# Optimization experiments

Measured on AMD Instinct MI355X. Metric: run time of the kernel, lower is better.

## Reference

```python
import jax, jax.numpy as jnp
import numpy as np

D = 128
SCALE = 1.0 / np.sqrt(D)  # scalar_value


def setup_inputs() -> dict:
    key = jax.random.key(0)
    k1, k2, k3 = jax.random.split(key, 3)
    B, N, S = 2, 16, 2048
    q = jax.random.normal(k1, (B, N, S, D), dtype=jnp.float32)
    k = jax.random.normal(k2, (B, N, S, D), dtype=jnp.float32)
    v = jax.random.normal(k3, (B, N, S, D), dtype=jnp.float32)
    return {"q": q, "k": k, "v": v}


def reference(q, k, v):
    # BNSD layout. scores = scale * Q K^T, causal mask, softmax with
    # explicit max/sum tracking (golden for NPU fusion attention).
    s1, s2 = q.shape[2], k.shape[2]
    scores = jnp.einsum('bnsd,bntd->bnst', q, k) * SCALE
    # generate_attn_mask: causal (lower-triangular kept), masked -> -inf
    causal = jnp.triu(jnp.ones((s1, s2), dtype=bool), k=1)
    scores = jnp.where(causal, -jnp.inf, scores)
    softmax_max = jnp.max(scores, axis=-1, keepdims=True)          # [B,N,S,1]
    exp_scores = jnp.exp(scores - softmax_max)
    softmax_sum = jnp.sum(exp_scores, axis=-1, keepdims=True)      # [B,N,S,1]
    softmax_res = exp_scores / softmax_sum
    out = jnp.einsum('bnst,bntd->bnsd', softmax_res, v)
    # NPU golden repeats stats x8 along last dim
    return (out,
            jnp.tile(softmax_max, (1, 1, 1, 8)),
            jnp.tile(softmax_sum, (1, 1, 1, 8)))
```

## Files before the change

kernel.cpp:

```cpp
#include <hip/hip_runtime.h>
#include <math.h>
#include <stdint.h>

#define D_DIM 128
#define SEQ 2048
#define NHEADS 32
#define BC 64
#define SCALE 0.08838834764831843f
#define IMG_U16 24576

typedef short bf16x8 __attribute__((ext_vector_type(8)));
typedef float f32x4 __attribute__((ext_vector_type(4)));

union Frag { uint32_t u[4]; bf16x8 v; unsigned short s[8]; };
union Pack8 { unsigned short s[8]; uint4 q; };

__device__ __forceinline__ uint32_t fbits(float x) { return __builtin_bit_cast(uint32_t, x); }
__device__ __forceinline__ float bbits(uint32_t u) { return __builtin_bit_cast(float, u); }
__device__ __forceinline__ unsigned short bf16_rne(float x) {
    uint32_t u = fbits(x);
    u += 0x7FFFu + ((u >> 16) & 1u);
    return (unsigned short)(u >> 16);
}
__device__ __forceinline__ void split2(float a, float b, uint32_t& hp, uint32_t& lp) {
    uint32_t ua = fbits(a) & 0xFFFF0000u, ub = fbits(b) & 0xFFFF0000u;
    float la = a - bbits(ua), lb = b - bbits(ub);
    hp = (ua >> 16) | ub;
    lp = (fbits(la) >> 16) | (fbits(lb) & 0xFFFF0000u);
}

__device__ __forceinline__ void gl_lds16(const unsigned short* g, unsigned short* l) {
    __builtin_amdgcn_global_load_lds(
        (const __attribute__((address_space(1))) uint32_t*)g,
        (__attribute__((address_space(3))) uint32_t*)l, 16, 0, 0);
}

__global__ __launch_bounds__(256) void cvt_kv(
    const float* __restrict__ k, const float* __restrict__ v, unsigned short* __restrict__ ws)
{
    const int b = blockIdx.x;
    const int h = b >> 5, jt = b & 31;
    const int t = (int)threadIdx.x;
    unsigned short* img = ws + (size_t)b * IMG_U16;
    const float* kp = k + ((size_t)h * SEQ + jt * 64) * D_DIM;
    const float* vp = v + ((size_t)h * SEQ + jt * 64) * D_DIM;

    #pragma unroll
    for (int u = 0; u < 4; ++u) {
        int idx = u * 256 + t;
        int n = idx >> 4, kc8 = idx & 15;
        float e[8];
        *(float4*)(e)     = *(const float4*)(kp + (size_t)n * D_DIM + kc8 * 8);
        *(float4*)(e + 4) = *(const float4*)(kp + (size_t)n * D_DIM + kc8 * 8 + 4);
        uint32_t hp[4], lp[4];
        #pragma unroll
        for (int j = 0; j < 4; ++j) split2(e[2 * j], e[2 * j + 1], hp[j], lp[j]);
        int off = n * 128 + ((kc8 ^ (n & 7)) * 8);
        *(uint4*)(img + off)        = make_uint4(hp[0], hp[1], hp[2], hp[3]);
        *(uint4*)(img + 8192 + off) = make_uint4(lp[0], lp[1], lp[2], lp[3]);
    }
    #pragma unroll
    for (int u = 0; u < 4; ++u) {
        int idx = u * 256 + t;
        int d = idx >> 3, cc = idx & 7;
        Pack8 p8;
        #pragma unroll
        for (int j = 0; j < 8; ++j)
            p8.s[j] = bf16_rne(vp[(size_t)(cc * 8 + j) * D_DIM + d]);
        int off = d * 64 + ((cc ^ (d & 7)) * 8);
        *(uint4*)(img + 16384 + off) = p8.q;
    }
}

__global__ __launch_bounds__(512, 2) void fa_fwd3(
    const float* __restrict__ q, const unsigned short* __restrict__ ws, float* __restrict__ out)
{
    __shared__ __align__(16) unsigned short Stage[2][IMG_U16];
    __shared__ __align__(16) unsigned short Pbs[128 * 64];

    const int x = blockIdx.x;
    const int it = 15 - (x >> 5);
    const int h = x & 31;

    const int t    = (int)threadIdx.x;
    const int wb   = t >> 6;
    const int lane = t & 63;
    const int ln   = lane & 15;
    const int qd   = lane >> 4;

    const unsigned short* wsh = ws + (size_t)(h * 32) * IMG_U16;
    float* out_o = out;
    float* out_m = out + (size_t)NHEADS * SEQ * D_DIM;
    float* out_l = out_m + (size_t)NHEADS * SEQ * 8;

    const int qrow0 = it * 128 + wb * 16;

    {
        const unsigned short* g = wsh + wb * 3072 + lane * 8;
        unsigned short* l = &Stage[0][wb * 3072];
        #pragma unroll
        for (int i = 0; i < 6; ++i) gl_lds16(g + i * 512, l + i * 512);
    }

    Frag Qh[4], Ql[4];
    {
        const float* qp = q + ((size_t)h * SEQ + qrow0 + ln) * D_DIM;
        #pragma unroll
        for (int kc = 0; kc < 4; ++kc) {
            const int kb = kc * 32 + qd * 8;
            float e[8];
            *(float4*)(e)     = *(const float4*)(qp + kb);
            *(float4*)(e + 4) = *(const float4*)(qp + kb + 4);
            #pragma unroll
            for (int j = 0; j < 4; ++j)
                split2(e[2 * j], e[2 * j + 1], Qh[kc].u[j], Ql[kc].u[j]);
        }
    }

    f32x4 accO[8];
    float m_r[4], l_r[4];
    #pragma unroll
    for (int nd = 0; nd < 8; ++nd) accO[nd] = (f32x4){0.f, 0.f, 0.f, 0.f};
    #pragma unroll
    for (int r = 0; r < 4; ++r) { m_r[r] = -INFINITY; l_r[r] = 0.f; }

    const int jt_end = 2 * it + 1;
    for (int jt = 0; jt <= jt_end; ++jt) {
        const int c0 = jt * BC;
        __syncthreads();

        if (jt < jt_end) {
            const unsigned short* g = wsh + (size_t)(jt + 1) * IMG_U16 + wb * 3072 + lane * 8;
            unsigned short* l = &Stage[(jt + 1) & 1][wb * 3072];
            #pragma unroll
            for (int i = 0; i < 6; ++i) gl_lds16(g + i * 512, l + i * 512);
        }

        const unsigned short* Khs = Stage[jt & 1];
        const unsigned short* Kls = Khs + 8192;
        const unsigned short* Vhs = Khs + 16384;

        if (c0 <= qrow0 + 15) {
            f32x4 accS[4];
            #pragma unroll
            for (int nt = 0; nt < 4; ++nt) accS[nt] = (f32x4){0.f, 0.f, 0.f, 0.f};
            #pragma unroll
            for (int kc = 0; kc < 4; ++kc) {
                #pragma unroll
                for (int nt = 0; nt < 4; ++nt) {
                    int n = nt * 16 + ln;
                    int off = n * 128 + (((kc * 4 + qd) ^ (n & 7)) * 8);
                    Frag Bh, Bl;
                    Bh.v = *(const bf16x8*)(Khs + off);
                    Bl.v = *(const bf16x8*)(Kls + off);
                    f32x4 c = accS[nt];
                    c = __builtin_amdgcn_mfma_f32_16x16x32_bf16(Qh[kc].v, Bh.v, c, 0, 0, 0);
                    c = __builtin_amdgcn_mfma_f32_16x16x32_bf16(Qh[kc].v, Bl.v, c, 0, 0, 0);
                    c = __builtin_amdgcn_mfma_f32_16x16x32_bf16(Ql[kc].v, Bh.v, c, 0, 0, 0);
                    accS[nt] = c;
                }
            }
            #pragma unroll
            for (int r = 0; r < 4; ++r) {
                const int rowg = qrow0 + qd * 4 + r;
                float sv[4], mx = -INFINITY;
                #pragma unroll
                for (int nt = 0; nt < 4; ++nt) {
                    float s = accS[nt][r] * SCALE;
                    if (c0 + nt * 16 + ln > rowg) s = -INFINITY;
                    sv[nt] = s; mx = fmaxf(mx, s);
                }
                #pragma unroll
                for (int off = 1; off < 16; off <<= 1) mx = fmaxf(mx, __shfl_xor(mx, off));
                const float mnew = fmaxf(m_r[r], mx);
                const float alpha = __expf(m_r[r] - mnew);
                float p[4], rs = 0.f;
                #pragma unroll
                for (int nt = 0; nt < 4; ++nt) { p[nt] = __expf(sv[nt] - mnew); rs += p[nt]; }
                #pragma unroll
                for (int off = 1; off < 16; off <<= 1) rs += __shfl_xor(rs, off);
                m_r[r] = mnew;
                l_r[r] = l_r[r] * alpha + rs;
                #pragma unroll
                for (int nd = 0; nd < 8; ++nd) accO[nd][r] *= alpha;
                const int R = wb * 16 + qd * 4 + r;
                #pragma unroll
                for (int nt = 0; nt < 4; ++nt) {
                    int c = nt * 16 + ln;
                    Pbs[R * 64 + (((c >> 3) ^ (R & 7)) * 8) + (c & 7)] = bf16_rne(p[nt]);
                }
            }
            #pragma unroll
            for (int kc2 = 0; kc2 < 2; ++kc2) {
                Frag Pf;
                const int R = wb * 16 + ln;
                Pf.v = *(const bf16x8*)(Pbs + R * 64 + (((kc2 * 4 + qd) ^ (R & 7)) * 8));
                #pragma unroll
                for (int nd = 0; nd < 8; ++nd) {
                    int dcol = nd * 16 + ln;
                    int voff = dcol * 64 + (((kc2 * 4 + qd) ^ (dcol & 7)) * 8);
                    Frag Vh2;
                    Vh2.v = *(const bf16x8*)(Vhs + voff);
                    accO[nd] = __builtin_amdgcn_mfma_f32_16x16x32_bf16(Pf.v, Vh2.v, accO[nd], 0, 0, 0);
                }
            }
        }
    }

    #pragma unroll
    for (int r = 0; r < 4; ++r) {
        const int rowg = qrow0 + qd * 4 + r;
        const float invl = 1.0f / l_r[r];
        float* op = out_o + (size_t)h * SEQ * D_DIM + (size_t)rowg * D_DIM;
        #pragma unroll
        for (int nd = 0; nd < 8; ++nd) op[nd * 16 + ln] = accO[nd][r] * invl;
        if (ln < 8) {
            size_t sb = ((size_t)h * SEQ + rowg) * 8 + ln;
            out_m[sb] = m_r[r];
            out_l[sb] = l_r[r];
        }
    }
}

__global__ __launch_bounds__(256, 2) void fa_fwd_fb(
    const float* __restrict__ q, const float* __restrict__ k,
    const float* __restrict__ v, float* __restrict__ out)
{
    __shared__ __align__(16) unsigned short Khs[64 * 128];
    __shared__ __align__(16) unsigned short Kls[64 * 128];
    __shared__ __align__(16) unsigned short Vhs[128 * 64];
    __shared__ __align__(16) unsigned short Vls[128 * 64];
    __shared__ __align__(16) unsigned short Pbs[128 * 64];

    const int x = blockIdx.x;
    const int y = x >> 3;
    const int s_idx = y & 15;
    const int h = (x & 7) * 4 + (y >> 4);
    const int it = (y < 32) ? (15 - s_idx) : s_idx;

    const int t = (int)threadIdx.x;
    const int wb = t >> 6, lane = t & 63, ln = lane & 15, qd = lane >> 4;

    const float* qh = q + (size_t)h * SEQ * D_DIM;
    const float* kh = k + (size_t)h * SEQ * D_DIM;
    const float* vh = v + (size_t)h * SEQ * D_DIM;
    float* out_o = out;
    float* out_m = out + (size_t)NHEADS * SEQ * D_DIM;
    float* out_l = out_m + (size_t)NHEADS * SEQ * 8;

    const int qrow0 = it * 128 + wb * 32;

    Frag Qh[2][4], Ql[2][4];
    #pragma unroll
    for (int mt = 0; mt < 2; ++mt) {
        const float* qp = qh + (size_t)(qrow0 + mt * 16 + ln) * D_DIM;
        #pragma unroll
        for (int kc = 0; kc < 4; ++kc) {
            const int kb = kc * 32 + qd * 8;
            float e[8];
            *(float4*)(e)     = *(const float4*)(qp + kb);
            *(float4*)(e + 4) = *(const float4*)(qp + kb + 4);
            #pragma unroll
            for (int j = 0; j < 4; ++j)
                split2(e[2 * j], e[2 * j + 1], Qh[mt][kc].u[j], Ql[mt][kc].u[j]);
        }
    }

    f32x4 accO[2][8];
    float m_r[2][4], l_r[2][4];
    #pragma unroll
    for (int mt = 0; mt < 2; ++mt) {
        #pragma unroll
        for (int nd = 0; nd < 8; ++nd) accO[mt][nd] = (f32x4){0.f, 0.f, 0.f, 0.f};
        #pragma unroll
        for (int r = 0; r < 4; ++r) { m_r[mt][r] = -INFINITY; l_r[mt][r] = 0.f; }
    }

    const int jt_end = 2 * it + 1;
    for (int jt = 0; jt <= jt_end; ++jt) {
        const int c0 = jt * BC;
        __syncthreads();
        #pragma unroll
        for (int itr = 0; itr < 8; ++itr) {
            int f = itr * 256 + t;
            int row = f >> 5, d4 = f & 31;
            float e[4];
            *(float4*)e = *(const float4*)(kh + (size_t)(c0 + row) * D_DIM + d4 * 4);
            uint32_t hp[2], lp[2];
            split2(e[0], e[1], hp[0], lp[0]);
            split2(e[2], e[3], hp[1], lp[1]);
            int off = row * 128 + (((d4 >> 1) ^ (row & 7)) * 8) + (d4 & 1) * 4;
            *(uint2*)(Khs + off) = make_uint2(hp[0], hp[1]);
            *(uint2*)(Kls + off) = make_uint2(lp[0], lp[1]);
        }
        #pragma unroll
        for (int uu = 0; uu < 4; ++uu) {
            int ug = wb * 4 + uu;
            int cc = ug >> 1, dh = ug & 1;
            int d = dh * 64 + lane;
            Frag fh, fl;
            #pragma unroll
            for (int j = 0; j < 8; j += 2) {
                float a = vh[(size_t)(c0 + cc * 8 + j) * D_DIM + d];
                float b = vh[(size_t)(c0 + cc * 8 + j + 1) * D_DIM + d];
                split2(a, b, fh.u[j >> 1], fl.u[j >> 1]);
            }
            int off = d * 64 + ((cc ^ (d & 7)) * 8);
            *(bf16x8*)(Vhs + off) = fh.v;
            *(bf16x8*)(Vls + off) = fl.v;
        }
        __syncthreads();

        if (c0 <= qrow0 + 31) {
            f32x4 accS[2][4];
            #pragma unroll
            for (int mt = 0; mt < 2; ++mt)
                #pragma unroll
                for (int nt = 0; nt < 4; ++nt) accS[mt][nt] = (f32x4){0.f, 0.f, 0.f, 0.f};
            #pragma unroll
            for (int kc = 0; kc < 4; ++kc) {
                #pragma unroll
                for (int ntp = 0; ntp < 4; ntp += 2) {
                    Frag Bh[2], Bl[2];
                    #pragma unroll
                    for (int e2 = 0; e2 < 2; ++e2) {
                        int n = (ntp + e2) * 16 + ln;
                        int off = n * 128 + (((kc * 4 + qd) ^ (n & 7)) * 8);
                        Bh[e2].v = *(const bf16x8*)(Khs + off);
                        Bl[e2].v = *(const bf16x8*)(Kls + off);
                    }
                    #pragma unroll
                    for (int mt = 0; mt < 2; ++mt)
                        #pragma unroll
                        for (int e2 = 0; e2 < 2; ++e2) {
                            f32x4 c = accS[mt][ntp + e2];
                            c = __builtin_amdgcn_mfma_f32_16x16x32_bf16(Qh[mt][kc].v, Bh[e2].v, c, 0, 0, 0);
                            c = __builtin_amdgcn_mfma_f32_16x16x32_bf16(Qh[mt][kc].v, Bl[e2].v, c, 0, 0, 0);
                            c = __builtin_amdgcn_mfma_f32_16x16x32_bf16(Ql[mt][kc].v, Bh[e2].v, c, 0, 0, 0);
                            accS[mt][ntp + e2] = c;
                        }
                }
            }
            #pragma unroll
            for (int mt = 0; mt < 2; ++mt) {
                #pragma unroll
                for (int r = 0; r < 4; ++r) {
                    const int rowg = qrow0 + mt * 16 + qd * 4 + r;
                    float sv[4], mx = -INFINITY;
                    #pragma unroll
                    for (int nt = 0; nt < 4; ++nt) {
                        float s = accS[mt][nt][r] * SCALE;
                        if (c0 + nt * 16 + ln > rowg) s = -INFINITY;
                        sv[nt] = s; mx = fmaxf(mx, s);
                    }
                    #pragma unroll
                    for (int off = 1; off < 16; off <<= 1) mx = fmaxf(mx, __shfl_xor(mx, off));
                    const float mnew = fmaxf(m_r[mt][r], mx);
                    const float alpha = __expf(m_r[mt][r] - mnew);
                    float p[4], rs = 0.f;
                    #pragma unroll
                    for (int nt = 0; nt < 4; ++nt) { p[nt] = __expf(sv[nt] - mnew); rs += p[nt]; }
                    #pragma unroll
                    for (int off = 1; off < 16; off <<= 1) rs += __shfl_xor(rs, off);
                    m_r[mt][r] = mnew;
                    l_r[mt][r] = l_r[mt][r] * alpha + rs;
                    #pragma unroll
                    for (int nd = 0; nd < 8; ++nd) accO[mt][nd][r] *= alpha;
                    const int R = wb * 32 + mt * 16 + qd * 4 + r;
                    #pragma unroll
                    for (int nt = 0; nt < 4; ++nt) {
                        int c = nt * 16 + ln;
                        Pbs[R * 64 + (((c >> 3) ^ (R & 7)) * 8) + (c & 7)] = bf16_rne(p[nt]);
                    }
                }
            }
            #pragma unroll
            for (int kc2 = 0; kc2 < 2; ++kc2) {
                Frag Pf[2];
                #pragma unroll
                for (int mt = 0; mt < 2; ++mt) {
                    int R = wb * 32 + mt * 16 + ln;
                    Pf[mt].v = *(const bf16x8*)(Pbs + R * 64 + (((kc2 * 4 + qd) ^ (R & 7)) * 8));
                }
                #pragma unroll
                for (int nd = 0; nd < 8; ++nd) {
                    int dcol = nd * 16 + ln;
                    int voff = dcol * 64 + (((kc2 * 4 + qd) ^ (dcol & 7)) * 8);
                    Frag Vh2, Vl2;
                    Vh2.v = *(const bf16x8*)(Vhs + voff);
                    Vl2.v = *(const bf16x8*)(Vls + voff);
                    #pragma unroll
                    for (int mt = 0; mt < 2; ++mt) {
                        f32x4 c = accO[mt][nd];
                        c = __builtin_amdgcn_mfma_f32_16x16x32_bf16(Pf[mt].v, Vh2.v, c, 0, 0, 0);
                        c = __builtin_amdgcn_mfma_f32_16x16x32_bf16(Pf[mt].v, Vl2.v, c, 0, 0, 0);
                        accO[mt][nd] = c;
                    }
                }
            }
        }
    }

    #pragma unroll
    for (int mt = 0; mt < 2; ++mt) {
        #pragma unroll
        for (int r = 0; r < 4; ++r) {
            const int rowg = qrow0 + mt * 16 + qd * 4 + r;
            const float invl = 1.0f / l_r[mt][r];
            float* op = out_o + (size_t)h * SEQ * D_DIM + (size_t)rowg * D_DIM;
            #pragma unroll
            for (int nd = 0; nd < 8; ++nd) op[nd * 16 + ln] = accO[mt][nd][r] * invl;
            if (ln < 8) {
                size_t sb = ((size_t)h * SEQ + rowg) * 8 + ln;
                out_m[sb] = m_r[mt][r];
                out_l[sb] = l_r[mt][r];
            }
        }
    }
}

extern "C" void kernel_launch(void* const* d_in, const int* in_sizes, int n_in,
                              void* d_out, int out_size, void* d_ws, size_t ws_size,
                              hipStream_t stream) {
    const float* q = (const float*)d_in[0];
    const float* k = (const float*)d_in[1];
    const float* v = (const float*)d_in[2];
    float* out = (float*)d_out;

    const size_t need = (size_t)1024 * IMG_U16 * sizeof(unsigned short);
    if (ws_size >= need) {
        unsigned short* ws = (unsigned short*)d_ws;
        cvt_kv<<<dim3(1024), dim3(256), 0, stream>>>(k, v, ws);
        fa_fwd3<<<dim3(512), dim3(512), 0, stream>>>(q, ws, out);
    } else {
        fa_fwd_fb<<<dim3(512), dim3(256), 0, stream>>>(q, k, v, out);
    }
}
```

Measured before the change: 246.2 us.

## Rework attention forward: 32 rows per wave, MFMA row sums, DPP max, LDS-transposed V

Each wave now handles two 16-row Q tiles, so every K/V fragment read from LDS feeds twice as many MFMAs, and the block shrinks to 256 threads. The K/V tile double buffer is dropped for a single buffer loaded synchronously with an extra barrier each step. Row sums now come from an MFMA against a ones vector instead of shuffle reductions, and the row max uses DPP. Query tiles are reordered so heavy and light causal blocks are interleaved. The V transpose in cvt_kv now goes through LDS so global reads are coalesced. The costs are more register pressure and no overlap between the K/V load and compute.

Measured after the change: 252.0 us. +2.4%, slower.

```diff
diff --git a/kernel.cpp b/kernel.cpp
--- a/kernel.cpp
+++ b/kernel.cpp
@@ -35,9 +35,23 @@
         (__attribute__((address_space(3))) uint32_t*)l, 16, 0, 0);
 }
 
+__device__ __forceinline__ float dpp_max16(float x) {
+    int y;
+    y = __builtin_amdgcn_update_dpp(0, __builtin_bit_cast(int, x), 0xB1, 0xF, 0xF, true);
+    x = fmaxf(x, __builtin_bit_cast(float, y));
+    y = __builtin_amdgcn_update_dpp(0, __builtin_bit_cast(int, x), 0x4E, 0xF, 0xF, true);
+    x = fmaxf(x, __builtin_bit_cast(float, y));
+    y = __builtin_amdgcn_update_dpp(0, __builtin_bit_cast(int, x), 0x141, 0xF, 0xF, true);
+    x = fmaxf(x, __builtin_bit_cast(float, y));
+    y = __builtin_amdgcn_update_dpp(0, __builtin_bit_cast(int, x), 0x140, 0xF, 0xF, true);
+    x = fmaxf(x, __builtin_bit_cast(float, y));
+    return x;
+}
+
 __global__ __launch_bounds__(256) void cvt_kv(
     const float* __restrict__ k, const float* __restrict__ v, unsigned short* __restrict__ ws)
 {
+    __shared__ float Ls[64 * 129];
     const int b = blockIdx.x;
     const int h = b >> 5, jt = b & 31;
     const int t = (int)threadIdx.x;
@@ -45,6 +59,14 @@
     const float* kp = k + ((size_t)h * SEQ + jt * 64) * D_DIM;
     const float* vp = v + ((size_t)h * SEQ + jt * 64) * D_DIM;
 
+    #pragma unroll
+    for (int it = 0; it < 8; ++it) {
+        int idx = it * 256 + t;
+        int row = idx >> 5, c4 = idx & 31;
+        float4 e = *(const float4*)(vp + (size_t)row * D_DIM + c4 * 4);
+        float* lp = Ls + row * 129 + c4 * 4;
+        lp[0] = e.x; lp[1] = e.y; lp[2] = e.z; lp[3] = e.w;
+    }
     #pragma unroll
     for (int u = 0; u < 4; ++u) {
         int idx = u * 256 + t;
@@ -59,6 +81,7 @@
         *(uint4*)(img + off)        = make_uint4(hp[0], hp[1], hp[2], hp[3]);
         *(uint4*)(img + 8192 + off) = make_uint4(lp[0], lp[1], lp[2], lp[3]);
     }
+    __syncthreads();
     #pragma unroll
     for (int u = 0; u < 4; ++u) {
         int idx = u * 256 + t;
@@ -66,21 +89,21 @@
         Pack8 p8;
         #pragma unroll
         for (int j = 0; j < 8; ++j)
-            p8.s[j] = bf16_rne(vp[(size_t)(cc * 8 + j) * D_DIM + d]);
-        int off = d * 64 + ((cc ^ (d & 7)) * 8);
-        *(uint4*)(img + 16384 + off) = p8.q;
-    }
-}
-
-__global__ __launch_bounds__(512, 2) void fa_fwd3(
+            p8.s[j] = bf16_rne(Ls[(cc * 8 + j) * 129 + d]);
+        *(uint4*)(img + 16384 + d * 64 + ((cc ^ (d & 7)) * 8)) = p8.q;
+    }
+}
+
+__global__ __launch_bounds__(256, 2) void fa_fwd4(
     const float* __restrict__ q, const unsigned short* __restrict__ ws, float* __restrict__ out)
 {
-    __shared__ __align__(16) unsigned short Stage[2][IMG_U16];
+    __shared__ __align__(16) unsigned short Stage[IMG_U16];
     __shared__ __align__(16) unsigned short Pbs[128 * 64];
 
     const int x = blockIdx.x;
-    const int it = 15 - (x >> 5);
     const int h = x & 31;
+    const int s = (x >> 5) & 7;
+    const int it = (x < 256) ? (15 - s) : s;
 
     const int t    = (int)threadIdx.x;
     const int wb   = t >> 6;
@@ -93,18 +116,12 @@
     float* out_m = out + (size_t)NHEADS * SEQ * D_DIM;
     float* out_l = out_m + (size_t)NHEADS * SEQ * 8;
 
-    const int qrow0 = it * 128 + wb * 16;
-
-    {
-        const unsigned short* g = wsh + wb * 3072 + lane * 8;
-        unsigned short* l = &Stage[0][wb * 3072];
-        #pragma unroll
-        for (int i = 0; i < 6; ++i) gl_lds16(g + i * 512, l + i * 512);
-    }
-
-    Frag Qh[4], Ql[4];
-    {
-        const float* qp = q + ((size_t)h * SEQ + qrow0 + ln) * D_DIM;
+    const int qrow0 = it * 128 + wb * 32;
+
+    Frag Qh[2][4], Ql[2][4];
+    #pragma unroll
+    for (int mt = 0; mt < 2; ++mt) {
+        const float* qp = q + ((size_t)h * SEQ + qrow0 + mt * 16 + ln) * D_DIM;
         #pragma unroll
         for (int kc = 0; kc < 4; ++kc) {
             const int kb = kc * 32 + qd * 8;
@@ -113,37 +130,48 @@
             *(float4*)(e + 4) = *(const float4*)(qp + kb + 4);
             #pragma unroll
             for (int j = 0; j < 4; ++j)
-                split2(e[2 * j], e[2 * j + 1], Qh[kc].u[j], Ql[kc].u[j]);
-        }
-    }
-
-    f32x4 accO[8];
-    float m_r[4], l_r[4];
-    #pragma unroll
-    for (int nd = 0; nd < 8; ++nd) accO[nd] = (f32x4){0.f, 0.f, 0.f, 0.f};
-    #pragma unroll
-    for (int r = 0; r < 4; ++r) { m_r[r] = -INFINITY; l_r[r] = 0.f; }
+                split2(e[2 * j], e[2 * j + 1], Qh[mt][kc].u[j], Ql[mt][kc].u[j]);
+        }
+    }
+
+    Frag Ones;
+    #pragma unroll
+    for (int j = 0; j < 4; ++j) Ones.u[j] = 0x3F803F80u;
+
+    f32x4 accO[2][8], accL[2];
+    float m_r[2][4];
+    #pragma unroll
+    for (int mt = 0; mt < 2; ++mt) {
+        #pragma unroll
+        for (int nd = 0; nd < 8; ++nd) accO[mt][nd] = (f32x4){0.f, 0.f, 0.f, 0.f};
+        accL[mt] = (f32x4){0.f, 0.f, 0.f, 0.f};
+        #pragma unroll
+        for (int r = 0; r < 4; ++r) m_r[mt][r] = -INFINITY;
+    }
 
     const int jt_end = 2 * it + 1;
     for (int jt = 0; jt <= jt_end; ++jt) {
         const int c0 = jt * BC;
         __syncthreads();
 
-        if (jt < jt_end) {
-            const unsigned short* g = wsh + (size_t)(jt + 1) * IMG_U16 + wb * 3072 + lane * 8;
-            unsigned short* l = &Stage[(jt + 1) & 1][wb * 3072];
-            #pragma unroll
-            for (int i = 0; i < 6; ++i) gl_lds16(g + i * 512, l + i * 512);
-        }
-
-        const unsigned short* Khs = Stage[jt & 1];
-        const unsigned short* Kls = Khs + 8192;
-        const unsigned short* Vhs = Khs + 16384;
-
-        if (c0 <= qrow0 + 15) {
-            f32x4 accS[4];
-            #pragma unroll
-            for (int nt = 0; nt < 4; ++nt) accS[nt] = (f32x4){0.f, 0.f, 0.f, 0.f};
+        {
+            const unsigned short* g = wsh + (size_t)jt * IMG_U16 + wb * 6144 + lane * 8;
+            unsigned short* l = &Stage[wb * 6144];
+            #pragma unroll
+            for (int i = 0; i < 12; ++i) gl_lds16(g + i * 512, l + i * 512);
+        }
+        __syncthreads();
+
+        const unsigned short* Khs = Stage;
+        const unsigned short* Kls = Stage + 8192;
+        const unsigned short* Vhs = Stage + 16384;
+
+        if (c0 <= qrow0 + 31) {
+            f32x4 accS[2][4];
+            #pragma unroll
+            for (int mt = 0; mt < 2; ++mt)
+                #pragma unroll
+                for (int nt = 0; nt < 4; ++nt) accS[mt][nt] = (f32x4){0.f, 0.f, 0.f, 0.f};
             #pragma unroll
             for (int kc = 0; kc < 4; ++kc) {
                 #pragma unroll
@@ -153,71 +181,80 @@
                     Frag Bh, Bl;
                     Bh.v = *(const bf16x8*)(Khs + off);
                     Bl.v = *(const bf16x8*)(Kls + off);
-                    f32x4 c = accS[nt];
-                    c = __builtin_amdgcn_mfma_f32_16x16x32_bf16(Qh[kc].v, Bh.v, c, 0, 0, 0);
-                    c = __builtin_amdgcn_mfma_f32_16x16x32_bf16(Qh[kc].v, Bl.v, c, 0, 0, 0);
-                    c = __builtin_amdgcn_mfma_f32_16x16x32_bf16(Ql[kc].v, Bh.v, c, 0, 0, 0);
-                    accS[nt] = c;
-                }
-            }
-            #pragma unroll
-            for (int r = 0; r < 4; ++r) {
-                const int rowg = qrow0 + qd * 4 + r;
-                float sv[4], mx = -INFINITY;
-                #pragma unroll
-                for (int nt = 0; nt < 4; ++nt) {
-                    float s = accS[nt][r] * SCALE;
-                    if (c0 + nt * 16 + ln > rowg) s = -INFINITY;
-                    sv[nt] = s; mx = fmaxf(mx, s);
-                }
-                #pragma unroll
-                for (int off = 1; off < 16; off <<= 1) mx = fmaxf(mx, __shfl_xor(mx, off));
-                const float mnew = fmaxf(m_r[r], mx);
-                const float alpha = __expf(m_r[r] - mnew);
-                float p[4], rs = 0.f;
-                #pragma unroll
-                for (int nt = 0; nt < 4; ++nt) { p[nt] = __expf(sv[nt] - mnew); rs += p[nt]; }
-                #pragma unroll
-                for (int off = 1; off < 16; off <<= 1) rs += __shfl_xor(rs, off);
-                m_r[r] = mnew;
-                l_r[r] = l_r[r] * alpha + rs;
-                #pragma unroll
-                for (int nd = 0; nd < 8; ++nd) accO[nd][r] *= alpha;
-                const int R = wb * 16 + qd * 4 + r;
-                #pragma unroll
-                for (int nt = 0; nt < 4; ++nt) {
-                    int c = nt * 16 + ln;
-                    Pbs[R * 64 + (((c >> 3) ^ (R & 7)) * 8) + (c & 7)] = bf16_rne(p[nt]);
+                    #pragma unroll
+                    for (int mt = 0; mt < 2; ++mt) {
+                        f32x4 c = accS[mt][nt];
+                        c = __builtin_amdgcn_mfma_f32_16x16x32_bf16(Qh[mt][kc].v, Bh.v, c, 0, 0, 0);
+                        c = __builtin_amdgcn_mfma_f32_16x16x32_bf16(Qh[mt][kc].v, Bl.v, c, 0, 0, 0);
+                        c = __builtin_amdgcn_mfma_f32_16x16x32_bf16(Ql[mt][kc].v, Bh.v, c, 0, 0, 0);
+                        accS[mt][nt] = c;
+                    }
+                }
+            }
+            #pragma unroll
+            for (int mt = 0; mt < 2; ++mt) {
+                #pragma unroll
+                for (int r = 0; r < 4; ++r) {
+                    const int rowg = qrow0 + mt * 16 + qd * 4 + r;
+                    float sv[4], mx = -INFINITY;
+                    #pragma unroll
+                    for (int nt = 0; nt < 4; ++nt) {
+                        float sc = accS[mt][nt][r] * SCALE;
+                        if (c0 + nt * 16 + ln > rowg) sc = -INFINITY;
+                        sv[nt] = sc; mx = fmaxf(mx, sc);
+                    }
+                    mx = dpp_max16(mx);
+                    const float mnew = fmaxf(m_r[mt][r], mx);
+                    const float alpha = __expf(m_r[mt][r] - mnew);
+                    m_r[mt][r] = mnew;
+                    accL[mt][r] *= alpha;
+                    #pragma unroll
+                    for (int nd = 0; nd < 8; ++nd) accO[mt][nd][r] *= alpha;
+                    const int R = wb * 32 + mt * 16 + qd * 4 + r;
+                    #pragma unroll
+                    for (int nt = 0; nt < 4; ++nt) {
+                        int c = nt * 16 + ln;
+                        Pbs[R * 64 + (((c >> 3) ^ (R & 7)) * 8) + (c & 7)] = bf16_rne(__expf(sv[nt] - mnew));
+                    }
                 }
             }
             #pragma unroll
             for (int kc2 = 0; kc2 < 2; ++kc2) {
-                Frag Pf;
-                const int R = wb * 16 + ln;
-                Pf.v = *(const bf16x8*)(Pbs + R * 64 + (((kc2 * 4 + qd) ^ (R & 7)) * 8));
+                Frag Pf[2];
+                #pragma unroll
+                for (int mt = 0; mt < 2; ++mt) {
+                    const int R = wb * 32 + mt * 16 + ln;
+                    Pf[mt].v = *(const bf16x8*)(Pbs + R * 64 + (((kc2 * 4 + qd) ^ (R & 7)) * 8));
+                    accL[mt] = __builtin_amdgcn_mfma_f32_16x16x32_bf16(Pf[mt].v, Ones.v, accL[mt], 0, 0, 0);
+                }
                 #pragma unroll
                 for (int nd = 0; nd < 8; ++nd) {
                     int dcol = nd * 16 + ln;
-                    int voff = dcol * 64 + (((kc2 * 4 + qd) ^ (dcol & 7)) * 8);
                     Frag Vh2;
-                    Vh2.v = *(const bf16x8*)(Vhs + voff);
-                    accO[nd] = __builtin_amdgcn_mfma_f32_16x16x32_bf16(Pf.v, Vh2.v, accO[nd], 0, 0, 0);
-                }
-            }
-        }
-    }
-
-    #pragma unroll
-    for (int r = 0; r < 4; ++r) {
-        const int rowg = qrow0 + qd * 4 + r;
-        const float invl = 1.0f / l_r[r];
-        float* op = out_o + (size_t)h * SEQ * D_DIM + (size_t)rowg * D_DIM;
-        #pragma unroll
-        for (int nd = 0; nd < 8; ++nd) op[nd * 16 + ln] = accO[nd][r] * invl;
-        if (ln < 8) {
-            size_t sb = ((size_t)h * SEQ + rowg) * 8 + ln;
-            out_m[sb] = m_r[r];
-            out_l[sb] = l_r[r];
+                    Vh2.v = *(const bf16x8*)(Vhs + dcol * 64 + (((kc2 * 4 + qd) ^ (dcol & 7)) * 8));
+                    #pragma unroll
+                    for (int mt = 0; mt < 2; ++mt)
+                        accO[mt][nd] = __builtin_amdgcn_mfma_f32_16x16x32_bf16(Pf[mt].v, Vh2.v, accO[mt][nd], 0, 0, 0);
+                }
+            }
+        }
+    }
+
+    #pragma unroll
+    for (int mt = 0; mt < 2; ++mt) {
+        #pragma unroll
+        for (int r = 0; r < 4; ++r) {
+            const int rowg = qrow0 + mt * 16 + qd * 4 + r;
+            const float lv = accL[mt][r];
+            const float invl = 1.0f / lv;
+            float* op = out_o + (size_t)h * SEQ * D_DIM + (size_t)rowg * D_DIM;
+            #pragma unroll
+            for (int nd = 0; nd < 8; ++nd) op[nd * 16 + ln] = accO[mt][nd][r] * invl;
+            if (ln < 8) {
+                size_t sb = ((size_t)h * SEQ + rowg) * 8 + ln;
+                out_m[sb] = m_r[mt][r];
+                out_l[sb] = lv;
+            }
         }
     }
 }
@@ -320,25 +357,20 @@
             #pragma unroll
             for (int kc = 0; kc < 4; ++kc) {
                 #pragma unroll
-                for (int ntp = 0; ntp < 4; ntp += 2) {
-                    Frag Bh[2], Bl[2];
-                    #pragma unroll
-                    for (int e2 = 0; e2 < 2; ++e2) {
-                        int n = (ntp + e2) * 16 + ln;
-                        int off = n * 128 + (((kc * 4 + qd) ^ (n & 7)) * 8);
-                        Bh[e2].v = *(const bf16x8*)(Khs + off);
-                        Bl[e2].v = *(const bf16x8*)(Kls + off);
-                    }
-                    #pragma unroll
-                    for (int mt = 0; mt < 2; ++mt)
-                        #pragma unroll
-                        for (int e2 = 0; e2 < 2; ++e2) {
-                            f32x4 c = accS[mt][ntp + e2];
-                            c = __builtin_amdgcn_mfma_f32_16x16x32_bf16(Qh[mt][kc].v, Bh[e2].v, c, 0, 0, 0);
-                            c = __builtin_amdgcn_mfma_f32_16x16x32_bf16(Qh[mt][kc].v, Bl[e2].v, c, 0, 0, 0);
-                            c = __builtin_amdgcn_mfma_f32_16x16x32_bf16(Ql[mt][kc].v, Bh[e2].v, c, 0, 0, 0);
-                            accS[mt][ntp + e2] = c;
-                        }
+                for (int nt = 0; nt < 4; ++nt) {
+                    int n = nt * 16 + ln;
+                    int off = n * 128 + (((kc * 4 + qd) ^ (n & 7)) * 8);
+                    Frag Bh, Bl;
+                    Bh.v = *(const bf16x8*)(Khs + off);
+                    Bl.v = *(const bf16x8*)(Kls + off);
+                    #pragma unroll
+                    for (int mt = 0; mt < 2; ++mt) {
+                        f32x4 c = accS[mt][nt];
+                        c = __builtin_amdgcn_mfma_f32_16x16x32_bf16(Qh[mt][kc].v, Bh.v, c, 0, 0, 0);
+                        c = __builtin_amdgcn_mfma_f32_16x16x32_bf16(Qh[mt][kc].v, Bl.v, c, 0, 0, 0);
+                        c = __builtin_amdgcn_mfma_f32_16x16x32_bf16(Ql[mt][kc].v, Bh.v, c, 0, 0, 0);
+                        accS[mt][nt] = c;
+                    }
                 }
             }
             #pragma unroll
@@ -349,9 +381,9 @@
                     float sv[4], mx = -INFINITY;
                     #pragma unroll
                     for (int nt = 0; nt < 4; ++nt) {
-                        float s = accS[mt][nt][r] * SCALE;
-                        if (c0 + nt * 16 + ln > rowg) s = -INFINITY;
-                        sv[nt] = s; mx = fmaxf(mx, s);
+                        float sc = accS[mt][nt][r] * SCALE;
+                        if (c0 + nt * 16 + ln > rowg) sc = -INFINITY;
+                        sv[nt] = sc; mx = fmaxf(mx, sc);
                     }
                     #pragma unroll
                     for (int off = 1; off < 16; off <<= 1) mx = fmaxf(mx, __shfl_xor(mx, off));
@@ -431,7 +463,7 @@
     if (ws_size >= need) {
         unsigned short* ws = (unsigned short*)d_ws;
         cvt_kv<<<dim3(1024), dim3(256), 0, stream>>>(k, v, ws);
-        fa_fwd3<<<dim3(512), dim3(512), 0, stream>>>(q, ws, out);
+        fa_fwd4<<<dim3(512), dim3(256), 0, stream>>>(q, ws, out);
     } else {
         fa_fwd_fb<<<dim3(512), dim3(256), 0, stream>>>(q, k, v, out);
     }
```
